# Kernel optimization log

Hardware: AMD Instinct MI355X
Metric: run time of the kernel (lower is better)

The kernel has to match this reference:

```python
import jax, jax.numpy as jnp
import numpy as np

B, T, I, H, L = 256, 2000, 80, 20, 2
G = 4 * H  # gates i,f,g,o (PyTorch order)


def _lstm_dir(xg, w_hh, reverse):
    # xg: [B, T, 4H] precomputed input-gate contributions (incl. bias)
    # w_hh: [H, 4H]
    xg_t = jnp.swapaxes(xg, 0, 1)  # [T, B, 4H]
    if reverse:
        xg_t = xg_t[::-1]

    def step(carry, g_x):
        h, c = carry
        gates = g_x + h @ w_hh  # [B, 4H]
        i, f, g, o = jnp.split(gates, 4, axis=-1)
        c = jax.nn.sigmoid(f) * c + jax.nn.sigmoid(i) * jnp.tanh(g)
        h = jax.nn.sigmoid(o) * jnp.tanh(c)
        return (h, c), h

    h0 = jnp.zeros((xg.shape[0], H), xg.dtype)
    _, hs = jax.lax.scan(step, (h0, h0), xg_t)  # hs: [T, B, H]
    if reverse:
        hs = hs[::-1]
    return jnp.swapaxes(hs, 0, 1)  # [B, T, H]


def _bilstm_layer(x, w_ih, w_hh, b):
    # x: [B, T, in], w_ih: [2, in, 4H], w_hh: [2, H, 4H], b: [2, 4H]
    out = []
    for d in range(2):
        xg = jnp.einsum('bti,ig->btg', x, w_ih[d]) + b[d]
        out.append(_lstm_dir(xg, w_hh[d], reverse=(d == 1)))
    return jnp.concatenate(out, axis=-1)  # [B, T, 2H]


def setup_inputs() -> dict:
    key = jax.random.key(0)
    ks = jax.random.split(key, 9)
    s = 1.0 / np.sqrt(H)
    u = lambda k, shp: jax.random.uniform(k, shp, jnp.float32, -s, s)
    return {
        'x': jax.random.normal(ks[0], (B, T, I), jnp.float32),
        'w_ih_l0': u(ks[1], (2, I, G)),
        'w_hh_l0': u(ks[2], (2, H, G)),
        'b_l0': u(ks[3], (2, G)),
        'w_ih_l1': u(ks[4], (2, 2 * H, G)),
        'w_hh_l1': u(ks[5], (2, H, G)),
        'b_l1': u(ks[6], (2, G)),
        'fc_w': u(ks[7], (1, 2 * H)),
        'fc_b': u(ks[8], (1,)),
    }


def reference(x, w_ih_l0, w_hh_l0, b_l0, w_ih_l1, w_hh_l1, b_l1, fc_w, fc_b):
    h = _bilstm_layer(x, w_ih_l0, w_hh_l0, b_l0)      # [B, T, 2H]
    h = _bilstm_layer(h, w_ih_l1, w_hh_l1, b_l1)      # [B, T, 2H]
    out = h @ fc_w.T + fc_b                           # [B, T, 1]
    return out.squeeze(-1)                            # [B, T]
```

## Files before the change

kernel.cpp:

```cpp
#include <hip/hip_runtime.h>
#include <math.h>

#define B_ 256
#define T_ 2000
#define I_ 80
#define H_ 20
#define G_ 80
#define M_ 512000

#define LOG2E 1.442695041f

typedef __attribute__((ext_vector_type(2))) float f32x2;

__device__ __forceinline__ f32x2 mk2(float a, float b) { f32x2 r; r.x = a; r.y = b; return r; }

template<int K>
__global__ __launch_bounds__(256) void gemm_xg(
    const float* __restrict__ X,
    const float* __restrict__ Wih,
    const float* __restrict__ Bias,
    float* __restrict__ XG,
    int M)
{
    constexpr int KC = 40;
    __shared__ float ws[KC][164];
    __shared__ float xs[KC][100];
    __shared__ float bs[160];

    const int tid  = threadIdx.x;
    const int row0 = blockIdx.x * 96;
    const int tx = tid % 20;
    const int ty = tid / 20;
    const bool run = (ty < 12);

    if (tid < 160) {
        int dd = (tid >= 80);
        int r = tid - 80 * dd;
        int j = r >> 2, g = r & 3;
        float sc = (g == 2) ? 2.0f * LOG2E : -LOG2E;
        bs[tid] = sc * Bias[dd * 80 + g * 20 + j];
    }

    int nrows = M - row0; if (nrows > 96) nrows = 96;

    float acc[8][8];
    bool first = true;

    for (int kc = 0; kc < K; kc += KC) {
        for (int idx = tid; idx < KC * 160; idx += 256) {
            int i = idx / 160, cc = idx - 160 * i;
            int dd = (cc >= 80), r = cc - 80 * dd;
            int j = r >> 2, g = r & 3;
            float sc = (g == 2) ? 2.0f * LOG2E : -LOG2E;
            ws[i][cc] = sc * Wih[(dd * K + kc + i) * 80 + g * 20 + j];
        }
        for (int i4 = tid; i4 < (96 * KC) / 4; i4 += 256) {
            int r = i4 / 10;
            int kk = (i4 - 10 * r) * 4;
            float4 v = make_float4(0.f, 0.f, 0.f, 0.f);
            if (r < nrows)
                v = *(const float4*)(X + (long long)(row0 + r) * K + kc + kk);
            xs[kk][r] = v.x; xs[kk + 1][r] = v.y; xs[kk + 2][r] = v.z; xs[kk + 3][r] = v.w;
        }
        __syncthreads();

        if (first) {
            first = false;
            float bv[8];
            #pragma unroll
            for (int cc = 0; cc < 8; ++cc) bv[cc] = bs[tx * 8 + cc];
            #pragma unroll
            for (int r = 0; r < 8; ++r)
                #pragma unroll
                for (int cc = 0; cc < 8; ++cc) acc[r][cc] = bv[cc];
        }

        if (run) {
            #pragma unroll 4
            for (int k = 0; k < KC; ++k) {
                float a[8], bb[8];
                *(float4*)&a[0]  = *(const float4*)&xs[k][ty * 8];
                *(float4*)&a[4]  = *(const float4*)&xs[k][ty * 8 + 4];
                *(float4*)&bb[0] = *(const float4*)&ws[k][tx * 8];
                *(float4*)&bb[4] = *(const float4*)&ws[k][tx * 8 + 4];
                #pragma unroll
                for (int r = 0; r < 8; ++r)
                    #pragma unroll
                    for (int cc = 0; cc < 8; ++cc)
                        acc[r][cc] = fmaf(a[r], bb[cc], acc[r][cc]);
            }
        }
        __syncthreads();
    }

    if (run) {
        #pragma unroll
        for (int r = 0; r < 8; ++r) {
            int row = row0 + ty * 8 + r;
            if (row < M) {
                float* dst = XG + (long long)row * 160 + tx * 8;
                *(float4*)(dst)     = *(float4*)&acc[r][0];
                *(float4*)(dst + 4) = *(float4*)&acc[r][4];
            }
        }
    }
}

__global__ __launch_bounds__(256) void gemm_xg_tA(
    const float* __restrict__ H0t,
    const float* __restrict__ Wih,
    const float* __restrict__ Bias,
    float* __restrict__ XG,
    int T)
{
    constexpr int K = 40;
    __shared__ float ws[K][164];
    __shared__ float xs[K][100];
    __shared__ float bs[160];

    const int tid = threadIdx.x;
    const int bb  = blockIdx.x / 21;
    const int tc  = blockIdx.x % 21;
    const int t0  = tc * 96;
    const int tx  = tid % 20;
    const int ty  = tid / 20;
    const bool run = (ty < 12);

    if (tid < 160) {
        int dd = (tid >= 80);
        int r = tid - 80 * dd;
        int j = r >> 2, g = r & 3;
        float sc = (g == 2) ? 2.0f * LOG2E : -LOG2E;
        bs[tid] = sc * Bias[dd * 80 + g * 20 + j];
    }

    int nrows = T - t0; if (nrows > 96) nrows = 96;

    for (int idx = tid; idx < K * 160; idx += 256) {
        int i = idx / 160, cc = idx - 160 * i;
        int dd = (cc >= 80), r = cc - 80 * dd;
        int j = r >> 2, g = r & 3;
        float sc = (g == 2) ? 2.0f * LOG2E : -LOG2E;
        ws[i][cc] = sc * Wih[(dd * K + i) * 80 + g * 20 + j];
    }
    for (int i4 = tid; i4 < K * 24; i4 += 256) {
        int k = i4 / 24;
        int r = (i4 - 24 * k) * 4;
        float4 v = make_float4(0.f, 0.f, 0.f, 0.f);
        if (r < nrows)
            v = *(const float4*)(H0t + ((long long)bb * 40 + k) * T + t0 + r);
        *(float4*)&xs[k][r] = v;
    }
    __syncthreads();

    float acc[8][8];
    {
        float bv[8];
        #pragma unroll
        for (int cc = 0; cc < 8; ++cc) bv[cc] = bs[tx * 8 + cc];
        #pragma unroll
        for (int r = 0; r < 8; ++r)
            #pragma unroll
            for (int cc = 0; cc < 8; ++cc) acc[r][cc] = bv[cc];
    }

    if (run) {
        #pragma unroll 4
        for (int k = 0; k < K; ++k) {
            float a[8], bb2[8];
            *(float4*)&a[0]   = *(const float4*)&xs[k][ty * 8];
            *(float4*)&a[4]   = *(const float4*)&xs[k][ty * 8 + 4];
            *(float4*)&bb2[0] = *(const float4*)&ws[k][tx * 8];
            *(float4*)&bb2[4] = *(const float4*)&ws[k][tx * 8 + 4];
            #pragma unroll
            for (int r = 0; r < 8; ++r)
                #pragma unroll
                for (int cc = 0; cc < 8; ++cc)
                    acc[r][cc] = fmaf(a[r], bb2[cc], acc[r][cc]);
        }

        #pragma unroll
        for (int r = 0; r < 8; ++r) {
            int rr = ty * 8 + r;
            if (rr < nrows) {
                long long row = (long long)bb * T + t0 + rr;
                float* dst = XG + row * 160 + tx * 8;
                *(float4*)(dst)     = *(float4*)&acc[r][0];
                *(float4*)(dst + 4) = *(float4*)&acc[r][4];
            }
        }
    }
}

__attribute__((amdgpu_waves_per_eu(1, 1)))
__global__ __launch_bounds__(64) void lstm_scan(
    const float* __restrict__ xg,
    const float* __restrict__ w_hh,
    float* __restrict__ h_out,
    int T)
{
    const int bd   = blockIdx.x;
    const int b    = bd >> 1;
    const int d    = bd & 1;
    const int lane = threadIdx.x & 63;
    const int j    = lane & 31;
    const bool act_lane = (lane < H_);
    const int jj   = (j < H_) ? j : 0;
    const bool isB = (d == 1);

    f32x2 w[4][10];
    const float* wb = w_hh + d * (H_ * G_);
    #pragma unroll
    for (int g = 0; g < 4; ++g) {
        const float sc = (g == 2) ? 2.0f * LOG2E : -LOG2E;
        #pragma unroll
        for (int i = 0; i < 10; ++i)
            w[g][i] = mk2(sc * wb[(2 * i) * G_ + g * 20 + jj],
                          sc * wb[(2 * i + 1) * G_ + g * 20 + jj]);
    }

    float sh[20];
    #pragma unroll
    for (int k = 0; k < 20; ++k) sh[k] = 0.f;
    float c = 0.f;

    const int t0    = isB ? (T - 1) : 0;
    const int rstep = isB ? -160 : 160;
    const float* pf = xg + ((long long)(b * T + t0) * 2 + d) * 80 + 4 * jj;

    float* hp = h_out + ((long long)b * 40 + d * 20 + jj) * T + (isB ? T - 4 : 0);
    const int hgstep = isB ? -4 : 4;

    constexpr int PF = 8;
    float4 px[PF];
    #pragma unroll
    for (int s = 0; s < PF; ++s) { px[s] = *(const float4*)pf; pf += rstep; }

    float hq0 = 0.f, hq1 = 0.f, hq2 = 0.f, hq3 = 0.f;

    for (int tb = 0; tb < T; tb += PF) {
        #pragma unroll
        for (int s = 0; s < PF; ++s) {
            const float4 v = px[s];
            px[s] = *(const float4*)pf; pf += rstep;

            f32x2 aL[4], aH[4];
            aL[0] = mk2(v.x, 0.f); aL[1] = mk2(v.y, 0.f);
            aL[2] = mk2(v.z, 0.f); aL[3] = mk2(v.w, 0.f);
            #pragma unroll
            for (int g = 0; g < 4; ++g) aH[g] = mk2(0.f, 0.f);

            #pragma unroll
            for (int i = 0; i < 5; ++i) {
                const f32x2 hlo = mk2(sh[2 * i],      sh[2 * i + 1]);
                const f32x2 hhi = mk2(sh[10 + 2 * i], sh[11 + 2 * i]);
                #pragma unroll
                for (int g = 0; g < 4; ++g) {
                    aL[g] = __builtin_elementwise_fma(w[g][i],     hlo, aL[g]);
                    aH[g] = __builtin_elementwise_fma(w[g][i + 5], hhi, aH[g]);
                }
            }
            float m[4];
            #pragma unroll
            for (int g = 0; g < 4; ++g) {
                const f32x2 t2 = aL[g] + aH[g];
                m[g] = t2.x + t2.y;
            }

            const float gi = __builtin_amdgcn_rcpf(1.0f + __builtin_amdgcn_exp2f(m[0]));
            const float gf = __builtin_amdgcn_rcpf(1.0f + __builtin_amdgcn_exp2f(m[1]));
            const float gg = fmaf(-2.0f,
                __builtin_amdgcn_rcpf(1.0f + __builtin_amdgcn_exp2f(m[2])), 1.0f);
            const float go = __builtin_amdgcn_rcpf(1.0f + __builtin_amdgcn_exp2f(m[3]));

            c = fmaf(gf, c, gi * gg);
            const float th = fmaf(-2.0f,
                __builtin_amdgcn_rcpf(1.0f + __builtin_amdgcn_exp2f(2.0f * LOG2E * c)), 1.0f);
            const float hj = go * th;

            {
                const int p = s & 3;
                if (p == 0) hq0 = hj;
                else if (p == 1) hq1 = hj;
                else if (p == 2) hq2 = hj;
                else {
                    hq3 = hj;
                    float4 sv;
                    sv.x = isB ? hq3 : hq0;
                    sv.y = isB ? hq2 : hq1;
                    sv.z = isB ? hq1 : hq2;
                    sv.w = isB ? hq0 : hq3;
                    if (act_lane) *(float4*)hp = sv;
                    hp += hgstep;
                }
            }

            #pragma unroll
            for (int k = 0; k < 20; ++k)
                sh[k] = __uint_as_float(__builtin_amdgcn_readlane(__float_as_uint(hj), k));
        }
    }
}

__global__ __launch_bounds__(256) void fc_t(
    const float* __restrict__ H1t,
    const float* __restrict__ Wf,
    const float* __restrict__ Bf,
    float* __restrict__ Out,
    int T)
{
    const int b   = blockIdx.x;
    const int t   = blockIdx.y * 1024 + threadIdx.x * 4;
    if (t > T - 4) return;

    const float bias = Bf[0];
    float4 acc = make_float4(bias, bias, bias, bias);
    const float* base = H1t + (long long)b * 40 * T + t;
    #pragma unroll 8
    for (int u = 0; u < 40; ++u) {
        const float wv = Wf[u];
        const float4 hv = *(const float4*)(base + (long long)u * T);
        acc.x = fmaf(hv.x, wv, acc.x);
        acc.y = fmaf(hv.y, wv, acc.y);
        acc.z = fmaf(hv.z, wv, acc.z);
        acc.w = fmaf(hv.w, wv, acc.w);
    }
    *(float4*)(Out + (long long)b * T + t) = acc;
}

extern "C" void kernel_launch(void* const* d_in, const int* in_sizes, int n_in,
                              void* d_out, int out_size, void* d_ws, size_t ws_size,
                              hipStream_t stream) {
    const float* x     = (const float*)d_in[0];
    const float* wih0  = (const float*)d_in[1];
    const float* whh0  = (const float*)d_in[2];
    const float* b0    = (const float*)d_in[3];
    const float* wih1  = (const float*)d_in[4];
    const float* whh1  = (const float*)d_in[5];
    const float* b1    = (const float*)d_in[6];
    const float* fcw   = (const float*)d_in[7];
    const float* fcb   = (const float*)d_in[8];
    float* out = (float*)d_out;

    float* ws = (float*)d_ws;
    float* xg  = ws + 2048;
    float* h0t = xg + 81920000LL + 2048;
    float* h1t = h0t + 20480000LL;

    const int M = M_;
    const int gemm_grid = (M + 95) / 96;

    gemm_xg<80><<<dim3(gemm_grid), dim3(256), 0, stream>>>(x, wih0, b0, xg, M);
    lstm_scan<<<dim3(B_ * 2), dim3(64), 0, stream>>>(xg, whh0, h0t, T_);
    gemm_xg_tA<<<dim3(B_ * 21), dim3(256), 0, stream>>>(h0t, wih1, b1, xg, T_);
    lstm_scan<<<dim3(B_ * 2), dim3(64), 0, stream>>>(xg, whh1, h1t, T_);
    fc_t<<<dim3(B_, 2), dim3(256), 0, stream>>>(h1t, fcw, fcb, out, T_);
}
```

Baseline: 1.533 ms.

## Split LSTM gate matvec across both wave halves with cross-half lane swap

The recurrent scan previously used only 20 of 64 lanes, each computing all four gates. Now the upper half-wave computes gates g and o while the lower half computes i and f. The two halves exchange their sigmoid results with a permlane32 swap, or ds_bpermute as a fallback. This halves the per-lane FMA chain and register weights on the serial critical path, at the cost of a cross-lane exchange every timestep.

```diff
diff --git a/kernel.cpp b/kernel.cpp
--- a/kernel.cpp
+++ b/kernel.cpp
@@ -11,8 +11,19 @@
 #define LOG2E 1.442695041f
 
 typedef __attribute__((ext_vector_type(2))) float f32x2;
+typedef __attribute__((ext_vector_type(2))) unsigned u32x2;
 
 __device__ __forceinline__ f32x2 mk2(float a, float b) { f32x2 r; r.x = a; r.y = b; return r; }
+
+__device__ __forceinline__ float swap_half(float x, int swapidx) {
+#if __has_builtin(__builtin_amdgcn_permlane32_swap)
+    u32x2 r = __builtin_amdgcn_permlane32_swap(__float_as_uint(x), __float_as_uint(x), false, false);
+    return __uint_as_float(r.y);
+#else
+    (void)0;
+    return __uint_as_float((unsigned)__builtin_amdgcn_ds_bpermute(swapidx, (int)__float_as_uint(x)));
+#endif
+}
 
 template<int K>
 __global__ __launch_bounds__(256) void gemm_xg(
@@ -203,20 +214,27 @@
     const int b    = bd >> 1;
     const int d    = bd & 1;
     const int lane = threadIdx.x & 63;
+    const int half = lane >> 5;
     const int j    = lane & 31;
     const bool act_lane = (lane < H_);
     const int jj   = (j < H_) ? j : 0;
     const bool isB = (d == 1);
 
-    f32x2 w[4][10];
+    const int swapidx = ((lane + 32) & 63) << 2;
+
+    const int gA = half ? 2 : 0;
+    const int gB = gA + 1;
+    const float scA = half ? (2.0f * LOG2E) : (-LOG2E);
+    const float scB = -LOG2E;
+
+    f32x2 wA[10], wB[10];
     const float* wb = w_hh + d * (H_ * G_);
     #pragma unroll
-    for (int g = 0; g < 4; ++g) {
-        const float sc = (g == 2) ? 2.0f * LOG2E : -LOG2E;
-        #pragma unroll
-        for (int i = 0; i < 10; ++i)
-            w[g][i] = mk2(sc * wb[(2 * i) * G_ + g * 20 + jj],
-                          sc * wb[(2 * i + 1) * G_ + g * 20 + jj]);
+    for (int i = 0; i < 10; ++i) {
+        wA[i] = mk2(scA * wb[(2 * i) * G_ + gA * 20 + jj],
+                    scA * wb[(2 * i + 1) * G_ + gA * 20 + jj]);
+        wB[i] = mk2(scB * wb[(2 * i) * G_ + gB * 20 + jj],
+                    scB * wb[(2 * i + 1) * G_ + gB * 20 + jj]);
     }
 
     float sh[20];
@@ -226,57 +244,53 @@
 
     const int t0    = isB ? (T - 1) : 0;
     const int rstep = isB ? -160 : 160;
-    const float* pf = xg + ((long long)(b * T + t0) * 2 + d) * 80 + 4 * jj;
+    const float* pf = xg + ((long long)(b * T + t0) * 2 + d) * 80 + 4 * jj + 2 * half;
 
     float* hp = h_out + ((long long)b * 40 + d * 20 + jj) * T + (isB ? T - 4 : 0);
     const int hgstep = isB ? -4 : 4;
 
     constexpr int PF = 8;
-    float4 px[PF];
+    f32x2 px[PF];
     #pragma unroll
-    for (int s = 0; s < PF; ++s) { px[s] = *(const float4*)pf; pf += rstep; }
+    for (int s = 0; s < PF; ++s) { px[s] = *(const f32x2*)pf; pf += rstep; }
 
     float hq0 = 0.f, hq1 = 0.f, hq2 = 0.f, hq3 = 0.f;
 
     for (int tb = 0; tb < T; tb += PF) {
         #pragma unroll
         for (int s = 0; s < PF; ++s) {
-            const float4 v = px[s];
-            px[s] = *(const float4*)pf; pf += rstep;
-
-            f32x2 aL[4], aH[4];
-            aL[0] = mk2(v.x, 0.f); aL[1] = mk2(v.y, 0.f);
-            aL[2] = mk2(v.z, 0.f); aL[3] = mk2(v.w, 0.f);
-            #pragma unroll
-            for (int g = 0; g < 4; ++g) aH[g] = mk2(0.f, 0.f);
-
+            const f32x2 v = px[s];
+            px[s] = *(const f32x2*)pf; pf += rstep;
+
+            f32x2 aA1 = mk2(v.x, 0.f);
+            f32x2 aA2 = mk2(0.f, 0.f);
+            f32x2 aB1 = mk2(v.y, 0.f);
+            f32x2 aB2 = mk2(0.f, 0.f);
             #pragma unroll
             for (int i = 0; i < 5; ++i) {
                 const f32x2 hlo = mk2(sh[2 * i],      sh[2 * i + 1]);
                 const f32x2 hhi = mk2(sh[10 + 2 * i], sh[11 + 2 * i]);
-                #pragma unroll
-                for (int g = 0; g < 4; ++g) {
-                    aL[g] = __builtin_elementwise_fma(w[g][i],     hlo, aL[g]);
-                    aH[g] = __builtin_elementwise_fma(w[g][i + 5], hhi, aH[g]);
-                }
-            }
-            float m[4];
-            #pragma unroll
-            for (int g = 0; g < 4; ++g) {
-                const f32x2 t2 = aL[g] + aH[g];
-                m[g] = t2.x + t2.y;
-            }
-
-            const float gi = __builtin_amdgcn_rcpf(1.0f + __builtin_amdgcn_exp2f(m[0]));
-            const float gf = __builtin_amdgcn_rcpf(1.0f + __builtin_amdgcn_exp2f(m[1]));
-            const float gg = fmaf(-2.0f,
-                __builtin_amdgcn_rcpf(1.0f + __builtin_amdgcn_exp2f(m[2])), 1.0f);
-            const float go = __builtin_amdgcn_rcpf(1.0f + __builtin_amdgcn_exp2f(m[3]));
-
-            c = fmaf(gf, c, gi * gg);
+                aA1 = __builtin_elementwise_fma(wA[i],     hlo, aA1);
+                aA2 = __builtin_elementwise_fma(wA[i + 5], hhi, aA2);
+                aB1 = __builtin_elementwise_fma(wB[i],     hlo, aB1);
+                aB2 = __builtin_elementwise_fma(wB[i + 5], hhi, aB2);
+            }
+            const f32x2 tA = aA1 + aA2;
+            const f32x2 tB = aB1 + aB2;
+            const float mA = tA.x + tA.y;
+            const float mB = tB.x + tB.y;
+
+            const float sA = __builtin_amdgcn_rcpf(1.0f + __builtin_amdgcn_exp2f(mA));
+            const float sB = __builtin_amdgcn_rcpf(1.0f + __builtin_amdgcn_exp2f(mB));
+
+            const float sAx = swap_half(sA, swapidx);
+            const float gox = swap_half(sB, swapidx);
+
+            const float gg = fmaf(-2.0f, sAx, 1.0f);
+            c = fmaf(sB, c, sA * gg);
             const float th = fmaf(-2.0f,
                 __builtin_amdgcn_rcpf(1.0f + __builtin_amdgcn_exp2f(2.0f * LOG2E * c)), 1.0f);
-            const float hj = go * th;
+            const float hj = gox * th;
 
             {
                 const int p = s & 3;
```

Result: faster. 1.343 ms (-12.4%).
